# Optimization experiments

Hardware: AMD Instinct MI355X
Metric: run time of the kernel (lower is better)

The kernel has to match this reference:

```python
import jax, jax.numpy as jnp
import numpy as np

N_ANCHORS = 25
N_CLASSES = 16
X_IMG = 296
Y_IMG = 296
OPLIST = ['conv','conv','MP','conv','conv','MP','conv','conv','conv','MP','conv','conv','conv','MP','conv','conv','conv']

def _size_list(s):
    out = [s]
    for op in OPLIST:
        out.append(out[-1] - 2 if op == 'conv' else out[-1] // 2)
    return out

XLIST = _size_list(X_IMG)  # ends at 7
YLIST = _size_list(Y_IMG)
FEAT = XLIST[-1]           # final feature-map size (7)
GRID = XLIST[-1] - 2       # anchor grid (5), source's xlist[-1]-2 convention
B, C = 2, 512


def setup_inputs() -> dict:
    key = jax.random.key(0)
    ks = jax.random.split(key, 12)
    D = C * 49
    return {
        'cfeats':   jax.random.normal(ks[0], (B, C, FEAT, FEAT), jnp.float32),
        'regcls':   jax.random.normal(ks[1], (B, 5, N_ANCHORS, GRID, GRID), jnp.float32) * 0.5,
        'wanchors': jax.random.uniform(ks[2], (N_ANCHORS, GRID, GRID), jnp.float32, 16.0, 128.0),
        'hanchors': jax.random.uniform(ks[3], (N_ANCHORS, GRID, GRID), jnp.float32, 16.0, 128.0),
        'xanchors': jax.random.uniform(ks[4], (N_ANCHORS, GRID, GRID), jnp.float32, 0.0, float(X_IMG)),
        'yanchors': jax.random.uniform(ks[5], (N_ANCHORS, GRID, GRID), jnp.float32, 0.0, float(Y_IMG)),
        'w1': jax.random.normal(ks[6], (200, D), jnp.float32) * 0.02,
        'b1': jnp.zeros((200,), jnp.float32),
        'w2': jax.random.normal(ks[7], (100, 200), jnp.float32) * 0.02,
        'b2': jnp.zeros((100,), jnp.float32),
        'w3': jax.random.normal(ks[8], (N_CLASSES + 1, 100), jnp.float32) * 0.02,
        'b3': jnp.zeros((N_CLASSES + 1,), jnp.float32),
        'w4': jax.random.normal(ks[9], (4 * (N_CLASSES + 1), 100), jnp.float32) * 0.02,
        'b4': jnp.zeros((4 * (N_CLASSES + 1),), jnp.float32),
    }


def _forward(cfeats, regcls, wanchors, hanchors, xanchors, yanchors,
             w1, b1, w2, b2, w3, b3, w4, b4):
    Bq, Cq, Fq, _ = cfeats.shape
    A, G = N_ANCHORS, GRID
    # ---- anchor-box decode ----
    wreg = jnp.exp(regcls[:, 2]) * wanchors
    hreg = jnp.exp(regcls[:, 3]) * hanchors
    xreg = regcls[:, 0] * wanchors + xanchors
    yreg = regcls[:, 1] * hanchors + yanchors
    xis = xreg - wreg / 2.0
    yis = yreg - hreg / 2.0
    xfs = xreg + wreg / 2.0
    yfs = yreg + hreg / 2.0
    c0 = jnp.floor(jax.nn.relu(xis))
    c1 = jnp.floor(jax.nn.relu(yis))
    c2 = jnp.minimum(jnp.ceil(xfs), float(X_IMG - 1))
    c3 = jnp.maximum(jnp.ceil(yfs), float(Y_IMG - 1))  # (sic) max, as in source
    valid = (xis < float(X_IMG)) & (yis < float(Y_IMG)) & (xfs >= 0.0) & (yfs >= 0.0)
    c4 = jnp.where(valid, jax.nn.sigmoid(regcls[:, 4]), 0.0)
    # ---- track coords through the conv/MP stack ----
    for i, op in enumerate(OPLIST):
        if op == 'conv':
            c0 = jax.nn.relu(c0 - 1.0)
            c1 = jax.nn.relu(c1 - 1.0)
            c2 = jnp.minimum(c2, float(XLIST[i + 1] - 1))
            c3 = jnp.minimum(c3, float(YLIST[i + 1] - 1))
        else:
            c0 = jnp.floor(c0 / 2.0); c1 = jnp.floor(c1 / 2.0)
            c2 = jnp.floor(c2 / 2.0); c3 = jnp.floor(c3 / 2.0)
    N = A * G * G  # flatten (anchor, x, y) -> roi index, same order as source
    xi = c0.reshape(Bq, N).astype(jnp.int32)
    yi = c1.reshape(Bq, N).astype(jnp.int32)
    xf = c2.reshape(Bq, N).astype(jnp.int32)
    yf = c3.reshape(Bq, N).astype(jnp.int32)
    roi_on = c4.reshape(Bq, N) > 0.0
    # ---- 7x7 RoIPool (vectorized; bins partition [xi, xf+1) via floor boundaries) ----
    ii = jnp.arange(8, dtype=jnp.int32)
    wx = xf + 1 - xi
    wy = yf + 1 - yi
    bx = xi[:, :, None] + (ii * wx[:, :, None]) // 7  # [B,N,8]
    by = yi[:, :, None] + (ii * wy[:, :, None]) // 7
    xs = jnp.arange(Fq, dtype=jnp.int32)
    maskx = (xs[None, None, None, :] >= bx[:, :, :7, None]) & (xs[None, None, None, :] < bx[:, :, 1:, None])  # [B,N,7,F]
    masky = (xs[None, None, None, :] >= by[:, :, :7, None]) & (xs[None, None, None, :] < by[:, :, 1:, None])
    NEG = jnp.float32(-1e30)
    feats_sg = jax.lax.stop_gradient(cfeats)
    # stage 1: max over x per bin i  -> val1/arg1: [B,N,7,C,F]
    val1 = jnp.full((Bq, N, 7, Cq, Fq), NEG, jnp.float32)
    arg1 = jnp.zeros((Bq, N, 7, Cq, Fq), jnp.int32)
    for x in range(Fq):
        cand = jnp.where(maskx[:, :, :, x][..., None, None], feats_sg[:, None, None, :, x, :], NEG)
        upd = cand > val1
        val1 = jnp.where(upd, cand, val1)
        arg1 = jnp.where(upd, x, arg1)
    # stage 2: max over y per bin j  -> val2/arg2: [B,N,7,7,C]
    val2 = jnp.full((Bq, N, 7, 7, Cq), NEG, jnp.float32)
    arg2 = jnp.zeros((Bq, N, 7, 7, Cq), jnp.int32)
    for y in range(Fq):
        cand = jnp.where(masky[:, :, None, :, y][..., None], val1[:, :, :, None, :, y], NEG)
        upd = cand > val2
        val2 = jnp.where(upd, cand, val2)
        arg2 = jnp.where(upd, y, arg2)
    # recover x index of the per-bin argmax, then one differentiable gather
    argx = jnp.take_along_axis(arg1[:, :, :, None, :, :], arg2[..., None], axis=-1)[..., 0]  # [B,N,7,7,C]
    cell = argx * Fq + arg2
    feats_flat = cfeats.reshape(Bq, Cq, Fq * Fq)
    pooled = jnp.take_along_axis(feats_flat[:, None, None, None, :, :], cell[..., None], axis=-1)[..., 0]
    keep = (val2 > NEG * 0.5) & roi_on[:, :, None, None, None]
    pooled = jnp.where(keep, pooled, 0.0)  # [B,N,7,7,C]
    # layout [..., C*49] with 49 = 7*i + j, matching source
    pooled = jnp.transpose(pooled, (0, 1, 4, 2, 3)).reshape(Bq, A, G, G, Cq * 49)
    # ---- MLP head ----
    z = jax.nn.relu(pooled @ w1.T + b1)
    z = jax.nn.relu(z @ w2.T + b2)
    z1 = z @ w3.T + b3
    z2 = z @ w4.T + b4
    K = N_CLASSES + 1
    z3 = jnp.stack([z2[..., 0:K], z2[..., K:2 * K], z2[..., 2 * K:3 * K], z2[..., 3 * K:4 * K]], axis=1)
    return z1, z3


def reference(cfeats, regcls, wanchors, hanchors, xanchors, yanchors,
              w1, b1, w2, b2, w3, b3, w4, b4):
    return _forward(cfeats, regcls, wanchors, hanchors, xanchors, yanchors,
                    w1, b1, w2, b2, w3, b3, w4, b4)
```

## Files before the change

### kernel.cpp

```cpp
#include <hip/hip_runtime.h>
#include <cstdint>

using short8 = __attribute__((ext_vector_type(8))) short;
using f32x4  = __attribute__((ext_vector_type(4))) float;

__device__ __forceinline__ uint16_t f2bf(float x) {
    uint32_t u = __float_as_uint(x);
    uint32_t r = (u + 0x7FFFu + ((u >> 16) & 1u)) >> 16;
    return (uint16_t)r;
}
__device__ __forceinline__ int fdiv7(int a) {
    int q = a / 7;
    if ((a % 7 != 0) && (a < 0)) q--;
    return q;
}

__global__ void __launch_bounds__(256) k_prep(const float* __restrict__ regcls,
                                              const float* __restrict__ wan,
                                              const float* __restrict__ han,
                                              const float* __restrict__ xan,
                                              const float* __restrict__ yan,
                                              const float* __restrict__ cf,
                                              const float* __restrict__ w1,
                                              const float* __restrict__ w2,
                                              const float* __restrict__ w3,
                                              const float* __restrict__ w4,
                                              int8_t* __restrict__ cells,
                                              uint16_t* __restrict__ cfb,
                                              uint16_t* __restrict__ w1f,
                                              float* __restrict__ w2t,
                                              float* __restrict__ w34t) {
    __shared__ float lds[16 * 804];
    int blk = blockIdx.x;
    int t = threadIdx.x;

    if (blk < 5) {
        int r = blk * 256 + t;
        if (r >= 1250) return;
        int b = r / 625, n = r - b * 625;
        const float* rc = regcls + b * 3125 + n;
        float t0 = rc[0], t1 = rc[625], t2 = rc[1250], t3 = rc[1875];
        float wa = wan[n], ha = han[n], xa = xan[n], ya = yan[n];
        float wr = expf(t2) * wa, hr = expf(t3) * ha;
        float xr = t0 * wa + xa, yr = t1 * ha + ya;
        float xis = xr - wr * 0.5f, yis = yr - hr * 0.5f;
        float xfs = xr + wr * 0.5f, yfs = yr + hr * 0.5f;
        bool valid = (xis < 296.f) && (yis < 296.f) && (xfs >= 0.f) && (yfs >= 0.f);
        int c0 = (int)floorf(fmaxf(xis, 0.f));
        int c1 = (int)floorf(fmaxf(yis, 0.f));
        int c2 = (int)fminf(ceilf(xfs), 295.f);
        int c3 = (int)fmaxf(ceilf(yfs), 295.f);
        const int  XL1[17]    = {294,292,146,144,142,71,69,67,65,32,30,28,26,13,11,9,7};
        const bool ISCONV[17] = {1,1,0,1,1,0,1,1,1,0,1,1,1,0,1,1,1};
        #pragma unroll
        for (int i = 0; i < 17; i++) {
            if (ISCONV[i]) {
                c0 = max(c0 - 1, 0); c1 = max(c1 - 1, 0);
                c2 = min(c2, XL1[i] - 1); c3 = min(c3, XL1[i] - 1);
            } else {
                c0 >>= 1; c1 >>= 1; c2 >>= 1; c3 >>= 1;
            }
        }
        int xi = c0, yi = c1, xf = c2, yf = c3;
        int wx = xf + 1 - xi, wy = yf + 1 - yi;
        int bx[8], by[8];
        #pragma unroll
        for (int i = 0; i < 8; i++) { bx[i] = xi + fdiv7(i * wx); by[i] = yi + fdiv7(i * wy); }
        int8_t* cr = cells + r * 64;
        #pragma unroll
        for (int i = 0; i < 7; i++)
            #pragma unroll
            for (int j = 0; j < 7; j++) {
                bool ne = valid && (bx[i + 1] > bx[i]) && (by[j + 1] > by[j]);
                cr[i * 7 + j] = ne ? (int8_t)(bx[i] * 7 + by[j]) : (int8_t)(-1);
            }
    } else if (blk < 37) {
        int g = (blk - 5) * 256 + t;
        int b = g >> 12;
        int xy = (g >> 6) & 63;
        int c0 = (g & 63) * 8;
        uint32_t pk[4];
        if (xy < 49) {
            #pragma unroll
            for (int h = 0; h < 4; h++) {
                uint16_t lo = f2bf(cf[(b * 512 + c0 + 2 * h) * 49 + xy]);
                uint16_t hi = f2bf(cf[(b * 512 + c0 + 2 * h + 1) * 49 + xy]);
                pk[h] = (uint32_t)lo | ((uint32_t)hi << 16);
            }
        } else {
            pk[0] = pk[1] = pk[2] = pk[3] = 0;
        }
        ((uint4*)cfb)[(b * 64 + xy) * 64 + (g & 63)] = make_uint4(pk[0], pk[1], pk[2], pk[3]);
    } else if (blk < 175) {
        int g = (blk - 37) * 256 + t;
        if (g < 200 * 128) {
            int k = g >> 7, o = g & 127;
            w2t[g] = (o < 100) ? w2[o * 200 + k] : 0.f;
        }
        int u = g - 200 * 128;
        if (u >= 0 && u < 100 * 96) {
            int k = u / 96, o = u - k * 96;
            float v = 0.f;
            if (o < 17) v = w3[o * 100 + k];
            else if (o < 85) v = w4[(o - 17) * 100 + k];
            w34t[u] = v;
        }
    } else {
        int idx = blk - 175;
        int nt = idx % 13, ct = idx / 13;
        int kbase = ct * 784;
        #pragma unroll 4
        for (int r = 0; r < 16; r++) {
            int o = nt * 16 + r;
            if (t < 196) {
                float4 v = make_float4(0.f, 0.f, 0.f, 0.f);
                if (o < 200) v = ((const float4*)(w1 + (size_t)o * 25088 + kbase))[t];
                *(float4*)&lds[r * 804 + 4 * t] = v;
            }
        }
        __syncthreads();
        int kc = ct >> 1;
        int q0 = (ct & 1) * 2;
        int lsub = t & 31;
        int l = q0 * 16 + lsub;
        int rrow = lsub & 15;
        int clbase = (lsub >> 4) * 8;
        for (int binb = 0; binb < 49; binb += 8) {
            int bin = binb + (t >> 5);
            if (bin < 49) {
                uint32_t pk[4];
                #pragma unroll
                for (int h = 0; h < 4; h++) {
                    uint16_t lo = f2bf(lds[rrow * 804 + (clbase + 2 * h) * 49 + bin]);
                    uint16_t hi = f2bf(lds[rrow * 804 + (clbase + 2 * h + 1) * 49 + bin]);
                    pk[h] = (uint32_t)lo | ((uint32_t)hi << 16);
                }
                ((uint4*)w1f)[((bin * 16 + kc) * 13 + nt) * 64 + l] =
                    make_uint4(pk[0], pk[1], pk[2], pk[3]);
            }
        }
    }
}

__global__ void __launch_bounds__(256) k_qgemm(const uint16_t* __restrict__ cfb,
                                               const uint16_t* __restrict__ w1f,
                                               float* __restrict__ Q) {
    __shared__ uint4 bs[16 * 64];
    int bin = blockIdx.x, nt = blockIdx.y, b = blockIdx.z;
    int t = threadIdx.x;
    const uint4* bw = (const uint4*)w1f + (bin * 16 * 13 + nt) * 64;
    for (int i = t; i < 16 * 64; i += 256) {
        int kc = i >> 6, l = i & 63;
        bs[i] = bw[kc * 832 + l];
    }
    __syncthreads();
    int w = t >> 6, l = t & 63;
    int mt = w;
    int r16 = l & 15, quad = l >> 4;
    const uint4* ap = (const uint4*)cfb + (b * 64 + mt * 16 + r16) * 64 + quad;
    f32x4 acc = {0.f, 0.f, 0.f, 0.f};
    #pragma unroll
    for (int kc = 0; kc < 16; kc++) {
        uint4 av = ap[kc * 4];
        uint4 bv = bs[kc * 64 + l];
        short8 a8 = __builtin_bit_cast(short8, av);
        short8 b8 = __builtin_bit_cast(short8, bv);
        acc = __builtin_amdgcn_mfma_f32_16x16x32_bf16(a8, b8, acc, 0, 0, 0);
    }
    int o = nt * 16 + r16;
    int xybase = mt * 16 + quad * 4;
    float* qb = Q + ((size_t)(b * 49 + bin) * 49) * 208 + o;
    #pragma unroll
    for (int reg = 0; reg < 4; reg++) {
        int xy = xybase + reg;
        if (xy < 49) qb[xy * 208] = acc[reg];
    }
}

__global__ void __launch_bounds__(256) k_head(const int8_t* __restrict__ cells,
                                              const float* __restrict__ Q,
                                              const float* __restrict__ b1,
                                              const float* __restrict__ w2t,
                                              const float* __restrict__ b2,
                                              const float* __restrict__ w34t,
                                              const float* __restrict__ b3,
                                              const float* __restrict__ b4,
                                              float* __restrict__ out) {
    __shared__ float z1[200];
    __shared__ float z2[100];
    int r = blockIdx.x;
    int b = r / 625, n = r - b * 625;
    int t = threadIdx.x;
    const int8_t* cr = cells + r * 64;
    float s = 0.f;
    if (t < 208) {
        const float* qb = Q + (size_t)(b * 49) * 49 * 208 + t;
        for (int bin = 0; bin < 49; bin++) {
            int cv = cr[bin];
            if (cv >= 0) s += qb[(bin * 49 + cv) * 208];
        }
    }
    if (t < 200) z1[t] = fmaxf(s + b1[t], 0.f);
    __syncthreads();
    if (t < 100) {
        float a = b2[t];
        #pragma unroll 4
        for (int k = 0; k < 200; k++) a += z1[k] * w2t[k * 128 + t];
        z2[t] = fmaxf(a, 0.f);
    }
    __syncthreads();
    if (t < 85) {
        float a = (t < 17) ? b3[t] : b4[t - 17];
        #pragma unroll 4
        for (int k = 0; k < 100; k++) a += z2[k] * w34t[k * 96 + t];
        if (t < 17) {
            out[b * 10625 + n * 17 + t] = a;
        } else {
            int q = (t - 17) / 17, kk = (t - 17) - q * 17;
            out[21250 + b * 42500 + q * 10625 + n * 17 + kk] = a;
        }
    }
}

extern "C" void kernel_launch(void* const* d_in, const int* in_sizes, int n_in,
                              void* d_out, int out_size, void* d_ws, size_t ws_size,
                              hipStream_t stream) {
    const float* cfeats = (const float*)d_in[0];
    const float* regcls = (const float*)d_in[1];
    const float* wan    = (const float*)d_in[2];
    const float* han    = (const float*)d_in[3];
    const float* xan    = (const float*)d_in[4];
    const float* yan    = (const float*)d_in[5];
    const float* w1     = (const float*)d_in[6];
    const float* b1     = (const float*)d_in[7];
    const float* w2     = (const float*)d_in[8];
    const float* b2     = (const float*)d_in[9];
    const float* w3     = (const float*)d_in[10];
    const float* b3     = (const float*)d_in[11];
    const float* w4     = (const float*)d_in[12];
    const float* b4     = (const float*)d_in[13];

    char* ws = (char*)d_ws;
    int8_t*   cells = (int8_t*)ws;
    uint16_t* cfb   = (uint16_t*)(ws + 80000);
    uint16_t* w1f   = (uint16_t*)(ws + 211072);
    float*    Q     = (float*)(ws + 10647680);
    float*    w2t   = (float*)(ws + 14642944);
    float*    w34t  = (float*)(ws + 14745344);
    float*    out   = (float*)d_out;

    k_prep<<<dim3(591), dim3(256), 0, stream>>>(regcls, wan, han, xan, yan,
                                                cfeats, w1, w2, w3, w4,
                                                cells, cfb, w1f, w2t, w34t);
    k_qgemm<<<dim3(49, 13, 2), dim3(256), 0, stream>>>(cfb, w1f, Q);
    k_head<<<dim3(1250), dim3(256), 0, stream>>>(cells, Q, b1, w2t, b2, w34t, b3, b4, out);
}
```

Before: 150.3 us.

## Fuse prep, GEMM and head kernels into one cooperative persistent kernel

Merges the three separate launches into a single cooperative kernel of 640 persistent blocks that use grid-wide syncs between the prep, Q-GEMM and MLP-head phases. The GEMM and head phases loop over virtual block indices, and the phases share one shared-memory buffer. This is meant to remove the launch overhead and inter-kernel gaps of the three launches. In exchange it pays for grid-barrier costs and limits occupancy to what keeps every block co-resident, with 51 KB of LDS per block and launch bounds of 3 blocks per SM.

Measured after the change: 354.6 us. +136.0%, slower.

```diff
diff --git a/kernel.cpp b/kernel.cpp
--- a/kernel.cpp
+++ b/kernel.cpp
@@ -1,8 +1,13 @@
 #include <hip/hip_runtime.h>
+#include <hip/hip_cooperative_groups.h>
 #include <cstdint>
+
+namespace cg = cooperative_groups;
 
 using short8 = __attribute__((ext_vector_type(8))) short;
 using f32x4  = __attribute__((ext_vector_type(4))) float;
+
+#define NBLK 640
 
 __device__ __forceinline__ uint16_t f2bf(float x) {
     uint32_t u = __float_as_uint(x);
@@ -15,65 +20,70 @@
     return q;
 }
 
-__global__ void __launch_bounds__(256) k_prep(const float* __restrict__ regcls,
-                                              const float* __restrict__ wan,
-                                              const float* __restrict__ han,
-                                              const float* __restrict__ xan,
-                                              const float* __restrict__ yan,
-                                              const float* __restrict__ cf,
-                                              const float* __restrict__ w1,
-                                              const float* __restrict__ w2,
-                                              const float* __restrict__ w3,
-                                              const float* __restrict__ w4,
-                                              int8_t* __restrict__ cells,
-                                              uint16_t* __restrict__ cfb,
-                                              uint16_t* __restrict__ w1f,
-                                              float* __restrict__ w2t,
-                                              float* __restrict__ w34t) {
-    __shared__ float lds[16 * 804];
-    int blk = blockIdx.x;
-    int t = threadIdx.x;
+__global__ void __launch_bounds__(256, 3)
+k_all(const float* __restrict__ regcls,
+      const float* __restrict__ wan,  const float* __restrict__ han,
+      const float* __restrict__ xan,  const float* __restrict__ yan,
+      const float* __restrict__ cf,   const float* __restrict__ w1,
+      const float* __restrict__ w2,   const float* __restrict__ w3,
+      const float* __restrict__ w4,
+      const float* __restrict__ b1,   const float* __restrict__ b2,
+      const float* __restrict__ b3,   const float* __restrict__ b4,
+      int8_t* __restrict__ cells, uint16_t* __restrict__ cfb,
+      uint16_t* __restrict__ w1f, float* __restrict__ w2t,
+      float* __restrict__ w34t,  float* __restrict__ Q,
+      float* __restrict__ out) {
+    __shared__ __align__(16) char smraw[51456];
+    float* smf = (float*)smraw;
+    uint4* bs  = (uint4*)smraw;
+    float* z1  = (float*)smraw;
+    float* z2  = (float*)(smraw + 800);
+
+    cg::grid_group grid = cg::this_grid();
+    const int t   = threadIdx.x;
+    const int blk = blockIdx.x;
 
     if (blk < 5) {
         int r = blk * 256 + t;
-        if (r >= 1250) return;
-        int b = r / 625, n = r - b * 625;
-        const float* rc = regcls + b * 3125 + n;
-        float t0 = rc[0], t1 = rc[625], t2 = rc[1250], t3 = rc[1875];
-        float wa = wan[n], ha = han[n], xa = xan[n], ya = yan[n];
-        float wr = expf(t2) * wa, hr = expf(t3) * ha;
-        float xr = t0 * wa + xa, yr = t1 * ha + ya;
-        float xis = xr - wr * 0.5f, yis = yr - hr * 0.5f;
-        float xfs = xr + wr * 0.5f, yfs = yr + hr * 0.5f;
-        bool valid = (xis < 296.f) && (yis < 296.f) && (xfs >= 0.f) && (yfs >= 0.f);
-        int c0 = (int)floorf(fmaxf(xis, 0.f));
-        int c1 = (int)floorf(fmaxf(yis, 0.f));
-        int c2 = (int)fminf(ceilf(xfs), 295.f);
-        int c3 = (int)fmaxf(ceilf(yfs), 295.f);
-        const int  XL1[17]    = {294,292,146,144,142,71,69,67,65,32,30,28,26,13,11,9,7};
-        const bool ISCONV[17] = {1,1,0,1,1,0,1,1,1,0,1,1,1,0,1,1,1};
-        #pragma unroll
-        for (int i = 0; i < 17; i++) {
-            if (ISCONV[i]) {
-                c0 = max(c0 - 1, 0); c1 = max(c1 - 1, 0);
-                c2 = min(c2, XL1[i] - 1); c3 = min(c3, XL1[i] - 1);
-            } else {
-                c0 >>= 1; c1 >>= 1; c2 >>= 1; c3 >>= 1;
-            }
-        }
-        int xi = c0, yi = c1, xf = c2, yf = c3;
-        int wx = xf + 1 - xi, wy = yf + 1 - yi;
-        int bx[8], by[8];
-        #pragma unroll
-        for (int i = 0; i < 8; i++) { bx[i] = xi + fdiv7(i * wx); by[i] = yi + fdiv7(i * wy); }
-        int8_t* cr = cells + r * 64;
-        #pragma unroll
-        for (int i = 0; i < 7; i++)
-            #pragma unroll
-            for (int j = 0; j < 7; j++) {
-                bool ne = valid && (bx[i + 1] > bx[i]) && (by[j + 1] > by[j]);
-                cr[i * 7 + j] = ne ? (int8_t)(bx[i] * 7 + by[j]) : (int8_t)(-1);
-            }
+        if (r < 1250) {
+            int b = r / 625, n = r - b * 625;
+            const float* rc = regcls + b * 3125 + n;
+            float t0 = rc[0], t1 = rc[625], t2 = rc[1250], t3 = rc[1875];
+            float wa = wan[n], ha = han[n], xa = xan[n], ya = yan[n];
+            float wr = expf(t2) * wa, hr = expf(t3) * ha;
+            float xr = t0 * wa + xa, yr = t1 * ha + ya;
+            float xis = xr - wr * 0.5f, yis = yr - hr * 0.5f;
+            float xfs = xr + wr * 0.5f, yfs = yr + hr * 0.5f;
+            bool valid = (xis < 296.f) && (yis < 296.f) && (xfs >= 0.f) && (yfs >= 0.f);
+            int c0 = (int)floorf(fmaxf(xis, 0.f));
+            int c1 = (int)floorf(fmaxf(yis, 0.f));
+            int c2 = (int)fminf(ceilf(xfs), 295.f);
+            int c3 = (int)fmaxf(ceilf(yfs), 295.f);
+            const int  XL1[17]    = {294,292,146,144,142,71,69,67,65,32,30,28,26,13,11,9,7};
+            const bool ISCONV[17] = {1,1,0,1,1,0,1,1,1,0,1,1,1,0,1,1,1};
+            #pragma unroll
+            for (int i = 0; i < 17; i++) {
+                if (ISCONV[i]) {
+                    c0 = max(c0 - 1, 0); c1 = max(c1 - 1, 0);
+                    c2 = min(c2, XL1[i] - 1); c3 = min(c3, XL1[i] - 1);
+                } else {
+                    c0 >>= 1; c1 >>= 1; c2 >>= 1; c3 >>= 1;
+                }
+            }
+            int xi = c0, yi = c1, xf = c2, yf = c3;
+            int wx = xf + 1 - xi, wy = yf + 1 - yi;
+            int bx[8], by[8];
+            #pragma unroll
+            for (int i = 0; i < 8; i++) { bx[i] = xi + fdiv7(i * wx); by[i] = yi + fdiv7(i * wy); }
+            int8_t* cr = cells + r * 64;
+            #pragma unroll
+            for (int i = 0; i < 7; i++)
+                #pragma unroll
+                for (int j = 0; j < 7; j++) {
+                    bool ne = valid && (bx[i + 1] > bx[i]) && (by[j + 1] > by[j]);
+                    cr[i * 7 + j] = ne ? (int8_t)(bx[i] * 7 + by[j]) : (int8_t)(-1);
+                }
+        }
     } else if (blk < 37) {
         int g = (blk - 5) * 256 + t;
         int b = g >> 12;
@@ -105,7 +115,7 @@
             else if (o < 85) v = w4[(o - 17) * 100 + k];
             w34t[u] = v;
         }
-    } else {
+    } else if (blk < 591) {
         int idx = blk - 175;
         int nt = idx % 13, ct = idx / 13;
         int kbase = ct * 784;
@@ -115,7 +125,7 @@
             if (t < 196) {
                 float4 v = make_float4(0.f, 0.f, 0.f, 0.f);
                 if (o < 200) v = ((const float4*)(w1 + (size_t)o * 25088 + kbase))[t];
-                *(float4*)&lds[r * 804 + 4 * t] = v;
+                *(float4*)&smf[r * 804 + 4 * t] = v;
             }
         }
         __syncthreads();
@@ -131,8 +141,8 @@
                 uint32_t pk[4];
                 #pragma unroll
                 for (int h = 0; h < 4; h++) {
-                    uint16_t lo = f2bf(lds[rrow * 804 + (clbase + 2 * h) * 49 + bin]);
-                    uint16_t hi = f2bf(lds[rrow * 804 + (clbase + 2 * h + 1) * 49 + bin]);
+                    uint16_t lo = f2bf(smf[rrow * 804 + (clbase + 2 * h) * 49 + bin]);
+                    uint16_t hi = f2bf(smf[rrow * 804 + (clbase + 2 * h + 1) * 49 + bin]);
                     pk[h] = (uint32_t)lo | ((uint32_t)hi << 16);
                 }
                 ((uint4*)w1f)[((bin * 16 + kc) * 13 + nt) * 64 + l] =
@@ -140,85 +150,76 @@
             }
         }
     }
-}
-
-__global__ void __launch_bounds__(256) k_qgemm(const uint16_t* __restrict__ cfb,
-                                               const uint16_t* __restrict__ w1f,
-                                               float* __restrict__ Q) {
-    __shared__ uint4 bs[16 * 64];
-    int bin = blockIdx.x, nt = blockIdx.y, b = blockIdx.z;
-    int t = threadIdx.x;
-    const uint4* bw = (const uint4*)w1f + (bin * 16 * 13 + nt) * 64;
-    for (int i = t; i < 16 * 64; i += 256) {
-        int kc = i >> 6, l = i & 63;
-        bs[i] = bw[kc * 832 + l];
+
+    grid.sync();
+
+    for (int vb = blk; vb < 1274; vb += NBLK) {
+        int bin = vb % 49;
+        int rest = vb / 49;
+        int nt = rest % 13, b = rest / 13;
+        const uint4* bw = (const uint4*)w1f + (bin * 208 + nt) * 64;
+        for (int i = t; i < 16 * 64; i += 256) {
+            int kc = i >> 6, l = i & 63;
+            bs[i] = bw[kc * 832 + l];
+        }
+        __syncthreads();
+        int w = t >> 6, l = t & 63;
+        int r16 = l & 15, quad = l >> 4;
+        const uint4* ap = (const uint4*)cfb + (b * 64 + w * 16 + r16) * 64 + quad;
+        f32x4 acc = {0.f, 0.f, 0.f, 0.f};
+        #pragma unroll
+        for (int kc = 0; kc < 16; kc++) {
+            uint4 av = ap[kc * 4];
+            uint4 bv = bs[kc * 64 + l];
+            short8 a8 = __builtin_bit_cast(short8, av);
+            short8 b8 = __builtin_bit_cast(short8, bv);
+            acc = __builtin_amdgcn_mfma_f32_16x16x32_bf16(a8, b8, acc, 0, 0, 0);
+        }
+        int o = nt * 16 + r16;
+        int xybase = w * 16 + quad * 4;
+        float* qb = Q + ((size_t)(b * 49 + bin) * 49) * 208 + o;
+        #pragma unroll
+        for (int reg = 0; reg < 4; reg++) {
+            int xy = xybase + reg;
+            if (xy < 49) qb[xy * 208] = acc[reg];
+        }
+        __syncthreads();
     }
-    __syncthreads();
-    int w = t >> 6, l = t & 63;
-    int mt = w;
-    int r16 = l & 15, quad = l >> 4;
-    const uint4* ap = (const uint4*)cfb + (b * 64 + mt * 16 + r16) * 64 + quad;
-    f32x4 acc = {0.f, 0.f, 0.f, 0.f};
-    #pragma unroll
-    for (int kc = 0; kc < 16; kc++) {
-        uint4 av = ap[kc * 4];
-        uint4 bv = bs[kc * 64 + l];
-        short8 a8 = __builtin_bit_cast(short8, av);
-        short8 b8 = __builtin_bit_cast(short8, bv);
-        acc = __builtin_amdgcn_mfma_f32_16x16x32_bf16(a8, b8, acc, 0, 0, 0);
-    }
-    int o = nt * 16 + r16;
-    int xybase = mt * 16 + quad * 4;
-    float* qb = Q + ((size_t)(b * 49 + bin) * 49) * 208 + o;
-    #pragma unroll
-    for (int reg = 0; reg < 4; reg++) {
-        int xy = xybase + reg;
-        if (xy < 49) qb[xy * 208] = acc[reg];
-    }
-}
-
-__global__ void __launch_bounds__(256) k_head(const int8_t* __restrict__ cells,
-                                              const float* __restrict__ Q,
-                                              const float* __restrict__ b1,
-                                              const float* __restrict__ w2t,
-                                              const float* __restrict__ b2,
-                                              const float* __restrict__ w34t,
-                                              const float* __restrict__ b3,
-                                              const float* __restrict__ b4,
-                                              float* __restrict__ out) {
-    __shared__ float z1[200];
-    __shared__ float z2[100];
-    int r = blockIdx.x;
-    int b = r / 625, n = r - b * 625;
-    int t = threadIdx.x;
-    const int8_t* cr = cells + r * 64;
-    float s = 0.f;
-    if (t < 208) {
-        const float* qb = Q + (size_t)(b * 49) * 49 * 208 + t;
-        for (int bin = 0; bin < 49; bin++) {
-            int cv = cr[bin];
-            if (cv >= 0) s += qb[(bin * 49 + cv) * 208];
-        }
-    }
-    if (t < 200) z1[t] = fmaxf(s + b1[t], 0.f);
-    __syncthreads();
-    if (t < 100) {
-        float a = b2[t];
-        #pragma unroll 4
-        for (int k = 0; k < 200; k++) a += z1[k] * w2t[k * 128 + t];
-        z2[t] = fmaxf(a, 0.f);
-    }
-    __syncthreads();
-    if (t < 85) {
-        float a = (t < 17) ? b3[t] : b4[t - 17];
-        #pragma unroll 4
-        for (int k = 0; k < 100; k++) a += z2[k] * w34t[k * 96 + t];
-        if (t < 17) {
-            out[b * 10625 + n * 17 + t] = a;
-        } else {
-            int q = (t - 17) / 17, kk = (t - 17) - q * 17;
-            out[21250 + b * 42500 + q * 10625 + n * 17 + kk] = a;
-        }
+
+    grid.sync();
+
+    for (int vb = blk; vb < 1250; vb += NBLK) {
+        int b = vb / 625, n = vb - b * 625;
+        const int8_t* cr = cells + vb * 64;
+        float s = 0.f;
+        if (t < 208) {
+            const float* qb = Q + (size_t)(b * 49) * 49 * 208 + t;
+            for (int bin = 0; bin < 49; bin++) {
+                int cv = cr[bin];
+                if (cv >= 0) s += qb[(bin * 49 + cv) * 208];
+            }
+        }
+        if (t < 200) z1[t] = fmaxf(s + b1[t], 0.f);
+        __syncthreads();
+        if (t < 100) {
+            float a = b2[t];
+            #pragma unroll 4
+            for (int k = 0; k < 200; k++) a += z1[k] * w2t[k * 128 + t];
+            z2[t] = fmaxf(a, 0.f);
+        }
+        __syncthreads();
+        if (t < 85) {
+            float a = (t < 17) ? b3[t] : b4[t - 17];
+            #pragma unroll 4
+            for (int k = 0; k < 100; k++) a += z2[k] * w34t[k * 96 + t];
+            if (t < 17) {
+                out[b * 10625 + n * 17 + t] = a;
+            } else {
+                int q = (t - 17) / 17, kk = (t - 17) - q * 17;
+                out[21250 + b * 42500 + q * 10625 + n * 17 + kk] = a;
+            }
+        }
+        __syncthreads();
     }
 }
 
@@ -249,9 +250,12 @@
     float*    w34t  = (float*)(ws + 14745344);
     float*    out   = (float*)d_out;
 
-    k_prep<<<dim3(591), dim3(256), 0, stream>>>(regcls, wan, han, xan, yan,
-                                                cfeats, w1, w2, w3, w4,
-                                                cells, cfb, w1f, w2t, w34t);
-    k_qgemm<<<dim3(49, 13, 2), dim3(256), 0, stream>>>(cfb, w1f, Q);
-    k_head<<<dim3(1250), dim3(256), 0, stream>>>(cells, Q, b1, w2t, b2, w34t, b3, b4, out);
-}
+    void* args[] = {
+        (void*)&regcls, (void*)&wan, (void*)&han, (void*)&xan, (void*)&yan,
+        (void*)&cfeats, (void*)&w1,  (void*)&w2,  (void*)&w3,  (void*)&w4,
+        (void*)&b1, (void*)&b2, (void*)&b3, (void*)&b4,
+        (void*)&cells, (void*)&cfb, (void*)&w1f, (void*)&w2t, (void*)&w34t,
+        (void*)&Q, (void*)&out
+    };
+    hipLaunchCooperativeKernel((void*)k_all, dim3(NBLK), dim3(256), args, 0, stream);
+}
```
